# Kernel optimization log

Hardware: AMD Instinct MI355X
Metric: run time of the kernel (lower is better)

The kernel has to match this reference:

```python
import jax, jax.numpy as jnp
import numpy as np

BZ, K, D = 16384, 8192, 512


def setup_inputs() -> dict:
    key = jax.random.key(0)
    kx, ke = jax.random.split(key)
    x = jax.random.normal(kx, (BZ, D), dtype=jnp.float32)
    emb = jax.random.normal(ke, (K, D), dtype=jnp.float32)
    return {"x": x, "emb": emb}


def reference(x, emb):
    x2 = jnp.sum(x * x, axis=1, keepdims=True)           # (bz, 1)
    e2 = jnp.sum(emb * emb, axis=1)                      # (K,)
    dist = x2 + e2[None, :] - 2.0 * jnp.einsum('bd,kd->bk', x, emb)  # (bz, K)
    indices = jnp.argmin(dist, axis=-1)                  # (bz,)
    return jnp.take(emb, indices, axis=0)                # (bz, D)
```

## Files before the change

kernel.cpp:

```cpp
#include <hip/hip_runtime.h>
#include <cfloat>

#define BZ    16384
#define KTOT  8192
#define DD    512
#define KK    512
#define MARGIN 2.0f

typedef unsigned long long u64;
typedef unsigned int       u32;
typedef __attribute__((ext_vector_type(8))) short bf16x8;
typedef __attribute__((ext_vector_type(4))) short bf16x4;
typedef __attribute__((ext_vector_type(4))) float f32x4;

__device__ __forceinline__ u32 f2bf_rne(float f) {
    u32 b = __float_as_uint(f);
    return (b + 0x7FFFu + ((b >> 16) & 1u)) >> 16;
}

__device__ __forceinline__ u64 pack_key(float s, int idx) {
    u32 b   = __float_as_uint(s);
    u32 key = (b & 0x80000000u) ? ~b : (b | 0x80000000u);
    return ((u64)key << 13) | (u32)idx;
}
__device__ __forceinline__ float unpack_val(u64 k) {
    u32 key = (u32)(k >> 13);
    u32 b   = (key & 0x80000000u) ? (key ^ 0x80000000u) : ~key;
    return __uint_as_float(b);
}

__device__ __forceinline__ void gload16(const void* g, void* l) {
    __builtin_amdgcn_global_load_lds(
        (const __attribute__((address_space(1))) void*)g,
        (__attribute__((address_space(3))) void*)l, 16, 0, 0);
}

__global__ void cast_x_kernel(const float* __restrict__ x, ushort* __restrict__ Xs) {
    const size_t base = ((size_t)blockIdx.x * 256 + threadIdx.x) * 8;
    float4 f0 = *(const float4*)(x + base);
    float4 f1 = *(const float4*)(x + base + 4);
    float ff[8] = {f0.x, f0.y, f0.z, f0.w, f1.x, f1.y, f1.z, f1.w};
    bf16x8 vh;
#pragma unroll
    for (int j = 0; j < 8; ++j) vh[j] = (short)f2bf_rne(ff[j]);
    *(bf16x8*)(Xs + base) = vh;
}

__global__ void cast_e_e2_kernel(const float* __restrict__ emb,
                                 ushort* __restrict__ Es, float* __restrict__ e2) {
    const int row  = blockIdx.x * 4 + (threadIdx.x >> 6);
    const int lane = threadIdx.x & 63;
    const float4* p = reinterpret_cast<const float4*>(emb + (size_t)row * DD);
    float4 a = p[lane];
    float4 b = p[lane + 64];
    bf16x4 ha, hb;
    ha[0] = (short)f2bf_rne(a.x); ha[1] = (short)f2bf_rne(a.y);
    ha[2] = (short)f2bf_rne(a.z); ha[3] = (short)f2bf_rne(a.w);
    hb[0] = (short)f2bf_rne(b.x); hb[1] = (short)f2bf_rne(b.y);
    hb[2] = (short)f2bf_rne(b.z); hb[3] = (short)f2bf_rne(b.w);
    ushort* d = Es + (size_t)row * DD;
    *(bf16x4*)(d + lane * 4)       = ha;
    *(bf16x4*)(d + 256 + lane * 4) = hb;
    float s = a.x * a.x + a.y * a.y + a.z * a.z + a.w * a.w
            + b.x * b.x + b.y * b.y + b.z * b.z + b.w * b.w;
#pragma unroll
    for (int off = 32; off >= 1; off >>= 1) s += __shfl_down(s, off, 64);
    if (lane == 0) e2[row] = s;
}

__global__ __launch_bounds__(256) void screen_kernel(
    const ushort* __restrict__ Xs, const ushort* __restrict__ Es,
    const float* __restrict__ e2, u64* __restrict__ cand)
{
    __shared__ __align__(16) ushort As[128 * 32];
    __shared__ __align__(16) ushort Bs[128 * 32];

    const int tid = threadIdx.x;
    const int ns  = blockIdx.x & 7;
    const int rb  = blockIdx.x >> 3;
    const int m0  = rb * 128;
    const int wid = tid >> 6;
    const int l   = tid & 63;
    const int wr  = wid >> 1, wc = wid & 1;
    const int lhi = l >> 4,   llo = l & 15;

    const int sr0 = (wid * 2 + 0) * 16 + (l >> 2);
    const int sr1 = (wid * 2 + 1) * 16 + (l >> 2);
    const int sc  = (l & 3) * 8;

    u64 t2a[16], t2b[16];
#pragma unroll
    for (int i = 0; i < 16; ++i) { t2a[i] = ~0ull; t2b[i] = ~0ull; }

#pragma unroll 1
    for (int nt = 0; nt < 8; ++nt) {
        const int n0 = ns * 1024 + nt * 128;
        f32x4 acc[4][4];
#pragma unroll
        for (int m = 0; m < 4; ++m)
#pragma unroll
            for (int n = 0; n < 4; ++n) acc[m][n] = (f32x4)(0.f);

#pragma unroll 1
        for (int ks = 0; ks < 16; ++ks) {
            const int k0 = ks * 32;
            __syncthreads();
            gload16(Xs + (size_t)(m0 + sr0) * KK + k0 + sc, &As[(wid * 2 + 0) * 512]);
            gload16(Xs + (size_t)(m0 + sr1) * KK + k0 + sc, &As[(wid * 2 + 1) * 512]);
            gload16(Es + (size_t)(n0 + sr0) * KK + k0 + sc, &Bs[(wid * 2 + 0) * 512]);
            gload16(Es + (size_t)(n0 + sr1) * KK + k0 + sc, &Bs[(wid * 2 + 1) * 512]);
            __syncthreads();

            bf16x8 a[4], b[4];
#pragma unroll
            for (int m = 0; m < 4; ++m)
                a[m] = *(const bf16x8*)&As[(wr * 64 + m * 16 + llo) * 32 + lhi * 8];
#pragma unroll
            for (int n = 0; n < 4; ++n)
                b[n] = *(const bf16x8*)&Bs[(wc * 64 + n * 16 + llo) * 32 + lhi * 8];
#pragma unroll
            for (int m = 0; m < 4; ++m)
#pragma unroll
                for (int n = 0; n < 4; ++n)
                    acc[m][n] = __builtin_amdgcn_mfma_f32_16x16x32_bf16(
                        a[m], b[n], acc[m][n], 0, 0, 0);
        }

#pragma unroll
        for (int n = 0; n < 4; ++n) {
            const int col = n0 + wc * 64 + n * 16 + llo;
            const float ee = e2[col];
#pragma unroll
            for (int m = 0; m < 4; ++m)
#pragma unroll
                for (int r = 0; r < 4; ++r) {
                    float s = fmaf(-2.f, acc[m][n][r], ee);
                    u64 k = pack_key(s, col);
                    const int mr = m * 4 + r;
                    if (k < t2a[mr]) { t2b[mr] = t2a[mr]; t2a[mr] = k; }
                    else if (k < t2b[mr]) t2b[mr] = k;
                }
        }
    }

#pragma unroll
    for (int mr = 0; mr < 16; ++mr) {
        u64 a = t2a[mr], b = t2b[mr];
#pragma unroll
        for (int mask = 1; mask < 16; mask <<= 1) {
            u64 oa = __shfl_xor(a, mask, 64);
            u64 ob = __shfl_xor(b, mask, 64);
            u64 hi = a < oa ? oa : a;
            u64 lo2 = b < ob ? b : ob;
            a = a < oa ? a : oa;
            b = hi < lo2 ? hi : lo2;
        }
        if (llo == 0) {
            const int row = m0 + wr * 64 + (mr >> 2) * 16 + lhi * 4 + (mr & 3);
            cand[(size_t)row * 32 + ns * 4 + wc * 2 + 0] = a;
            cand[(size_t)row * 32 + ns * 4 + wc * 2 + 1] = b;
        }
    }
}

__global__ __launch_bounds__(256) void rescore_gather_kernel(
    const float* __restrict__ x, const float* __restrict__ emb,
    const float* __restrict__ e2, const u64* __restrict__ cand,
    float* __restrict__ out)
{
    const int tid = threadIdx.x;
    const int wid = tid >> 6, l = tid & 63;
    const int row = blockIdx.x * 4 + wid;

    u64 c = (l < 32) ? cand[(size_t)row * 32 + l] : ~0ull;
    u64 mn = c;
#pragma unroll
    for (int off = 32; off >= 1; off >>= 1) {
        u64 o = __shfl_xor(mn, off, 64);
        mn = o < mn ? o : mn;
    }
    const float vbest = unpack_val(mn);
    const float v = unpack_val(c);
    const bool amb = (l < 32) && (v <= vbest + MARGIN);
    u64 ball = __ballot(amb);

    int widx;
    if (__popcll(ball) <= 1) {
        widx = (int)(mn & 0x1FFFu);
    } else {
        u64 bestk = ~0ull;
        const float4* xp = (const float4*)(x + (size_t)row * DD);
        while (ball) {
            const int b = __ffsll((unsigned long long)ball) - 1;
            ball &= ball - 1;
            const int ib = __shfl((int)(c & 0x1FFFu), b, 64);
            const float4* ep = (const float4*)(emb + (size_t)ib * DD);
            float4 xa = xp[l],      ea = ep[l];
            float4 xb = xp[l + 64], eb = ep[l + 64];
            float s = xa.x * ea.x + xa.y * ea.y + xa.z * ea.z + xa.w * ea.w
                    + xb.x * eb.x + xb.y * eb.y + xb.z * eb.z + xb.w * eb.w;
#pragma unroll
            for (int off = 32; off >= 1; off >>= 1) s += __shfl_xor(s, off, 64);
            const float d = fmaf(-2.f, s, e2[ib]);
            u64 k = pack_key(d, ib);
            if (k < bestk) bestk = k;
        }
        widx = (int)(bestk & 0x1FFFu);
    }

    const float4* src = (const float4*)(emb + (size_t)widx * DD);
    float4* dst = (float4*)(out + (size_t)row * DD);
    dst[l]      = src[l];
    dst[l + 64] = src[l + 64];
}

#define BM 64
#define BN 64
#define BKf 32
#define NCHUNKf (DD / BKf)
#define NTILESf (KTOT / BN)
#define LDT 68

__global__ void e2_only_kernel(const float* __restrict__ emb, float* __restrict__ e2) {
    const int row  = blockIdx.x * 4 + (threadIdx.x >> 6);
    const int lane = threadIdx.x & 63;
    const float4* p = reinterpret_cast<const float4*>(emb + (size_t)row * DD);
    float4 a = p[lane];
    float4 b = p[lane + 64];
    float s = a.x * a.x + a.y * a.y + a.z * a.z + a.w * a.w
            + b.x * b.x + b.y * b.y + b.z * b.z + b.w * b.w;
#pragma unroll
    for (int off = 32; off >= 1; off >>= 1) s += __shfl_down(s, off, 64);
    if (lane == 0) e2[row] = s;
}

__global__ __launch_bounds__(256) void vq_argmin_kernel(
    const float* __restrict__ x, const float* __restrict__ emb,
    const float* __restrict__ e2, float* __restrict__ out)
{
    __shared__ __align__(16) float xs[2][BKf][LDT];
    __shared__ __align__(16) float es[2][BKf][LDT];
    __shared__ float redv[BM][17];
    __shared__ int   redi[BM][17];
    __shared__ int   idx_s[BM];

    const int tid = threadIdx.x;
    const int tx  = tid & 15;
    const int ty  = tid >> 4;
    const int m0  = blockIdx.x * BM;
    const int srow = tid >> 3;
    const int scol = (tid & 7) << 2;

    const float* xb0 = x + (size_t)(m0 + srow) * DD + scol;
    const float* xb1 = xb0 + (size_t)32 * DD;

    float best[4]; int bidx[4];
#pragma unroll
    for (int i = 0; i < 4; ++i) { best[i] = FLT_MAX; bidx[i] = 0; }

#pragma unroll 1
    for (int nt = 0; nt < NTILESf; ++nt) {
        const int n0 = nt * BN;
        const float* eb0 = emb + (size_t)(n0 + srow) * DD + scol;
        const float* eb1 = eb0 + (size_t)32 * DD;
        float acc[4][4];
#pragma unroll
        for (int i = 0; i < 4; ++i)
#pragma unroll
            for (int j = 0; j < 4; ++j) acc[i][j] = 0.f;
        {
            float4 xa = *(const float4*)(xb0);
            float4 xc = *(const float4*)(xb1);
            float4 ea = *(const float4*)(eb0);
            float4 ec = *(const float4*)(eb1);
#pragma unroll
            for (int i = 0; i < 4; ++i) {
                xs[0][scol + i][srow]      = ((const float*)&xa)[i];
                xs[0][scol + i][srow + 32] = ((const float*)&xc)[i];
                es[0][scol + i][srow]      = ((const float*)&ea)[i];
                es[0][scol + i][srow + 32] = ((const float*)&ec)[i];
            }
        }
        __syncthreads();
        int cur = 0;
#pragma unroll 1
        for (int kk = 1; kk < NCHUNKf; ++kk) {
            float4 nxa = *(const float4*)(xb0 + kk * BKf);
            float4 nxc = *(const float4*)(xb1 + kk * BKf);
            float4 nea = *(const float4*)(eb0 + kk * BKf);
            float4 nec = *(const float4*)(eb1 + kk * BKf);
#pragma unroll
            for (int k = 0; k < BKf; ++k) {
                float4 a = *(const float4*)(&xs[cur][k][ty * 4]);
                float4 b = *(const float4*)(&es[cur][k][tx * 4]);
                acc[0][0] += a.x * b.x; acc[0][1] += a.x * b.y; acc[0][2] += a.x * b.z; acc[0][3] += a.x * b.w;
                acc[1][0] += a.y * b.x; acc[1][1] += a.y * b.y; acc[1][2] += a.y * b.z; acc[1][3] += a.y * b.w;
                acc[2][0] += a.z * b.x; acc[2][1] += a.z * b.y; acc[2][2] += a.z * b.z; acc[2][3] += a.z * b.w;
                acc[3][0] += a.w * b.x; acc[3][1] += a.w * b.y; acc[3][2] += a.w * b.z; acc[3][3] += a.w * b.w;
            }
            const int nb = cur ^ 1;
#pragma unroll
            for (int i = 0; i < 4; ++i) {
                xs[nb][scol + i][srow]      = ((const float*)&nxa)[i];
                xs[nb][scol + i][srow + 32] = ((const float*)&nxc)[i];
                es[nb][scol + i][srow]      = ((const float*)&nea)[i];
                es[nb][scol + i][srow + 32] = ((const float*)&nec)[i];
            }
            __syncthreads();
            cur = nb;
        }
#pragma unroll
        for (int k = 0; k < BKf; ++k) {
            float4 a = *(const float4*)(&xs[cur][k][ty * 4]);
            float4 b = *(const float4*)(&es[cur][k][tx * 4]);
            acc[0][0] += a.x * b.x; acc[0][1] += a.x * b.y; acc[0][2] += a.x * b.z; acc[0][3] += a.x * b.w;
            acc[1][0] += a.y * b.x; acc[1][1] += a.y * b.y; acc[1][2] += a.y * b.z; acc[1][3] += a.y * b.w;
            acc[2][0] += a.z * b.x; acc[2][1] += a.z * b.y; acc[2][2] += a.z * b.z; acc[2][3] += a.z * b.w;
            acc[3][0] += a.w * b.x; acc[3][1] += a.w * b.y; acc[3][2] += a.w * b.z; acc[3][3] += a.w * b.w;
        }
#pragma unroll
        for (int j = 0; j < 4; ++j) {
            const int n  = n0 + tx * 4 + j;
            const float ee = e2[n];
#pragma unroll
            for (int i = 0; i < 4; ++i) {
                float s = ee - 2.0f * acc[i][j];
                if (s < best[i]) { best[i] = s; bidx[i] = n; }
            }
        }
    }
#pragma unroll
    for (int i = 0; i < 4; ++i) {
        redv[ty * 4 + i][tx] = best[i];
        redi[ty * 4 + i][tx] = bidx[i];
    }
    __syncthreads();
    if (tid < BM) {
        float bv = redv[tid][0];
        int   bi = redi[tid][0];
#pragma unroll
        for (int t = 1; t < 16; ++t) {
            float v  = redv[tid][t];
            int   ii = redi[tid][t];
            if (v < bv || (v == bv && ii < bi)) { bv = v; bi = ii; }
        }
        idx_s[tid] = bi;
    }
    __syncthreads();
    for (int c = tid; c < BM * (DD / 4); c += 256) {
        const int r   = c >> 7;
        const int col = (c & 127) << 2;
        const float4 vv = *(const float4*)(emb + (size_t)idx_s[r] * DD + col);
        *(float4*)(out + (size_t)(m0 + r) * DD + col) = vv;
    }
}

extern "C" void kernel_launch(void* const* d_in, const int* in_sizes, int n_in,
                              void* d_out, int out_size, void* d_ws, size_t ws_size,
                              hipStream_t stream) {
    const float* x   = (const float*)d_in[0];
    const float* emb = (const float*)d_in[1];
    float* out = (float*)d_out;

    const size_t XS_BYTES   = (size_t)BZ * KK * 2;
    const size_t ES_BYTES   = (size_t)KTOT * KK * 2;
    const size_t E2_BYTES   = (size_t)KTOT * 4;
    const size_t CAND_BYTES = (size_t)BZ * 32 * 8;
    const size_t NEEDED = XS_BYTES + ES_BYTES + E2_BYTES + CAND_BYTES;

    if (ws_size >= NEEDED) {
        char* base = (char*)d_ws;
        ushort* Xs = (ushort*)base;
        ushort* Es = (ushort*)(base + XS_BYTES);
        float*  e2 = (float*)(base + XS_BYTES + ES_BYTES);
        u64*  cand = (u64*)(base + XS_BYTES + ES_BYTES + E2_BYTES);

        cast_x_kernel<<<(BZ * DD) / (256 * 8), 256, 0, stream>>>(x, Xs);
        cast_e_e2_kernel<<<KTOT / 4, 256, 0, stream>>>(emb, Es, e2);
        screen_kernel<<<(BZ / 128) * 8, 256, 0, stream>>>(Xs, Es, e2, cand);
        rescore_gather_kernel<<<BZ / 4, 256, 0, stream>>>(x, emb, e2, cand, out);
    } else {
        float* e2 = (float*)d_ws;
        e2_only_kernel<<<KTOT / 4, 256, 0, stream>>>(emb, e2);
        vq_argmin_kernel<<<BZ / BM, 256, 0, stream>>>(x, emb, e2, out);
    }
}
```

Before: 379.3 us.

## Double-buffer LDS tiles and track top-2 with biased 32-bit keys

The screening GEMM now double-buffers the A/B LDS tiles. The next k-slice's global-to-LDS loads are issued while the current slice feeds the MFMAs, which leaves one barrier per step instead of two. The per-row top-2 tracking switches from 64-bit packed keys to 32-bit keys. A bias added to e2 keeps distances positive so raw float bits sort correctly, and the low 5 mantissa bits hold the tile position; the column is rebuilt after the cross-lane reduction. This cuts register pressure and compare cost in the epilogue. The mantissa truncation loses precision, so the rescore margin is widened to compensate, and a second e2 buffer is allocated in the workspace.

```diff
diff --git a/kernel.cpp b/kernel.cpp
--- a/kernel.cpp
+++ b/kernel.cpp
@@ -5,7 +5,8 @@
 #define KTOT  8192
 #define DD    512
 #define KK    512
-#define MARGIN 2.0f
+#define MARGIN 2.5f
+#define BIAS  16384.0f
 
 typedef unsigned long long u64;
 typedef unsigned int       u32;
@@ -24,9 +25,7 @@
     return ((u64)key << 13) | (u32)idx;
 }
 __device__ __forceinline__ float unpack_val(u64 k) {
-    u32 key = (u32)(k >> 13);
-    u32 b   = (key & 0x80000000u) ? (key ^ 0x80000000u) : ~key;
-    return __uint_as_float(b);
+    return __uint_as_float((u32)(k >> 13)) - BIAS;
 }
 
 __device__ __forceinline__ void gload16(const void* g, void* l) {
@@ -47,7 +46,8 @@
 }
 
 __global__ void cast_e_e2_kernel(const float* __restrict__ emb,
-                                 ushort* __restrict__ Es, float* __restrict__ e2) {
+                                 ushort* __restrict__ Es, float* __restrict__ e2,
+                                 float* __restrict__ e2b) {
     const int row  = blockIdx.x * 4 + (threadIdx.x >> 6);
     const int lane = threadIdx.x & 63;
     const float4* p = reinterpret_cast<const float4*>(emb + (size_t)row * DD);
@@ -65,15 +65,15 @@
             + b.x * b.x + b.y * b.y + b.z * b.z + b.w * b.w;
 #pragma unroll
     for (int off = 32; off >= 1; off >>= 1) s += __shfl_down(s, off, 64);
-    if (lane == 0) e2[row] = s;
+    if (lane == 0) { e2[row] = s; e2b[row] = s + BIAS; }
 }
 
 __global__ __launch_bounds__(256) void screen_kernel(
     const ushort* __restrict__ Xs, const ushort* __restrict__ Es,
-    const float* __restrict__ e2, u64* __restrict__ cand)
+    const float* __restrict__ e2b, u64* __restrict__ cand)
 {
-    __shared__ __align__(16) ushort As[128 * 32];
-    __shared__ __align__(16) ushort Bs[128 * 32];
+    __shared__ __align__(16) ushort As[2][128 * 32];
+    __shared__ __align__(16) ushort Bs[2][128 * 32];
 
     const int tid = threadIdx.x;
     const int ns  = blockIdx.x & 7;
@@ -88,9 +88,9 @@
     const int sr1 = (wid * 2 + 1) * 16 + (l >> 2);
     const int sc  = (l & 3) * 8;
 
-    u64 t2a[16], t2b[16];
-#pragma unroll
-    for (int i = 0; i < 16; ++i) { t2a[i] = ~0ull; t2b[i] = ~0ull; }
+    u32 ka[16], kb[16];
+#pragma unroll
+    for (int i = 0; i < 16; ++i) { ka[i] = 0xFFFFFFFFu; kb[i] = 0xFFFFFFFFu; }
 
 #pragma unroll 1
     for (int nt = 0; nt < 8; ++nt) {
@@ -101,23 +101,30 @@
 #pragma unroll
             for (int n = 0; n < 4; ++n) acc[m][n] = (f32x4)(0.f);
 
-#pragma unroll 1
+        gload16(Xs + (size_t)(m0 + sr0) * KK + sc, &As[0][(wid * 2 + 0) * 512]);
+        gload16(Xs + (size_t)(m0 + sr1) * KK + sc, &As[0][(wid * 2 + 1) * 512]);
+        gload16(Es + (size_t)(n0 + sr0) * KK + sc, &Bs[0][(wid * 2 + 0) * 512]);
+        gload16(Es + (size_t)(n0 + sr1) * KK + sc, &Bs[0][(wid * 2 + 1) * 512]);
+
+#pragma unroll 2
         for (int ks = 0; ks < 16; ++ks) {
-            const int k0 = ks * 32;
             __syncthreads();
-            gload16(Xs + (size_t)(m0 + sr0) * KK + k0 + sc, &As[(wid * 2 + 0) * 512]);
-            gload16(Xs + (size_t)(m0 + sr1) * KK + k0 + sc, &As[(wid * 2 + 1) * 512]);
-            gload16(Es + (size_t)(n0 + sr0) * KK + k0 + sc, &Bs[(wid * 2 + 0) * 512]);
-            gload16(Es + (size_t)(n0 + sr1) * KK + k0 + sc, &Bs[(wid * 2 + 1) * 512]);
-            __syncthreads();
-
+            const int cur = ks & 1;
+            if (ks < 15) {
+                const int k1 = (ks + 1) * 32;
+                const int nb = cur ^ 1;
+                gload16(Xs + (size_t)(m0 + sr0) * KK + k1 + sc, &As[nb][(wid * 2 + 0) * 512]);
+                gload16(Xs + (size_t)(m0 + sr1) * KK + k1 + sc, &As[nb][(wid * 2 + 1) * 512]);
+                gload16(Es + (size_t)(n0 + sr0) * KK + k1 + sc, &Bs[nb][(wid * 2 + 0) * 512]);
+                gload16(Es + (size_t)(n0 + sr1) * KK + k1 + sc, &Bs[nb][(wid * 2 + 1) * 512]);
+            }
             bf16x8 a[4], b[4];
 #pragma unroll
             for (int m = 0; m < 4; ++m)
-                a[m] = *(const bf16x8*)&As[(wr * 64 + m * 16 + llo) * 32 + lhi * 8];
+                a[m] = *(const bf16x8*)&As[cur][(wr * 64 + m * 16 + llo) * 32 + lhi * 8];
 #pragma unroll
             for (int n = 0; n < 4; ++n)
-                b[n] = *(const bf16x8*)&Bs[(wc * 64 + n * 16 + llo) * 32 + lhi * 8];
+                b[n] = *(const bf16x8*)&Bs[cur][(wc * 64 + n * 16 + llo) * 32 + lhi * 8];
 #pragma unroll
             for (int m = 0; m < 4; ++m)
 #pragma unroll
@@ -128,37 +135,45 @@
 
 #pragma unroll
         for (int n = 0; n < 4; ++n) {
-            const int col = n0 + wc * 64 + n * 16 + llo;
-            const float ee = e2[col];
+            const int col16 = n0 + wc * 64 + n * 16;
+            const float eeC = e2b[col16 + llo];
+            const u32 pos = (u32)(nt * 4 + n);
 #pragma unroll
             for (int m = 0; m < 4; ++m)
 #pragma unroll
                 for (int r = 0; r < 4; ++r) {
-                    float s = fmaf(-2.f, acc[m][n][r], ee);
-                    u64 k = pack_key(s, col);
+                    const float s = fmaf(-2.f, acc[m][n][r], eeC);
+                    const u32 k = (__float_as_uint(s) & 0xFFFFFFE0u) | pos;
                     const int mr = m * 4 + r;
-                    if (k < t2a[mr]) { t2b[mr] = t2a[mr]; t2a[mr] = k; }
-                    else if (k < t2b[mr]) t2b[mr] = k;
+                    const bool c2 = k < kb[mr];
+                    const bool c1 = k < ka[mr];
+                    kb[mr] = c1 ? ka[mr] : (c2 ? k : kb[mr]);
+                    ka[mr] = c1 ? k : ka[mr];
                 }
         }
     }
 
 #pragma unroll
     for (int mr = 0; mr < 16; ++mr) {
-        u64 a = t2a[mr], b = t2b[mr];
+        u64 a = ((u64)ka[mr] << 4) | (u32)llo;
+        u64 b = ((u64)kb[mr] << 4) | (u32)llo;
 #pragma unroll
         for (int mask = 1; mask < 16; mask <<= 1) {
             u64 oa = __shfl_xor(a, mask, 64);
             u64 ob = __shfl_xor(b, mask, 64);
-            u64 hi = a < oa ? oa : a;
+            u64 hi  = a < oa ? oa : a;
             u64 lo2 = b < ob ? b : ob;
             a = a < oa ? a : oa;
             b = hi < lo2 ? hi : lo2;
         }
         if (llo == 0) {
             const int row = m0 + wr * 64 + (mr >> 2) * 16 + lhi * 4 + (mr & 3);
-            cand[(size_t)row * 32 + ns * 4 + wc * 2 + 0] = a;
-            cand[(size_t)row * 32 + ns * 4 + wc * 2 + 1] = b;
+            const u32 k32a = (u32)(a >> 4), la = (u32)a & 15u, pa = k32a & 31u;
+            const u32 k32b = (u32)(b >> 4), lb = (u32)b & 15u, pb = k32b & 31u;
+            const u32 cola = (u32)(ns * 1024) + (pa >> 2) * 128 + (u32)(wc * 64) + (pa & 3u) * 16 + la;
+            const u32 colb = (u32)(ns * 1024) + (pb >> 2) * 128 + (u32)(wc * 64) + (pb & 3u) * 16 + lb;
+            cand[(size_t)row * 32 + ns * 4 + wc * 2 + 0] = ((u64)k32a << 13) | cola;
+            cand[(size_t)row * 32 + ns * 4 + wc * 2 + 1] = ((u64)k32b << 13) | colb;
         }
     }
 }
@@ -366,7 +381,7 @@
     const size_t ES_BYTES   = (size_t)KTOT * KK * 2;
     const size_t E2_BYTES   = (size_t)KTOT * 4;
     const size_t CAND_BYTES = (size_t)BZ * 32 * 8;
-    const size_t NEEDED = XS_BYTES + ES_BYTES + E2_BYTES + CAND_BYTES;
+    const size_t NEEDED = XS_BYTES + ES_BYTES + 2 * E2_BYTES + CAND_BYTES;
 
     if (ws_size >= NEEDED) {
         char* base = (char*)d_ws;
@@ -374,10 +389,11 @@
         ushort* Es = (ushort*)(base + XS_BYTES);
         float*  e2 = (float*)(base + XS_BYTES + ES_BYTES);
         u64*  cand = (u64*)(base + XS_BYTES + ES_BYTES + E2_BYTES);
+        float* e2b = (float*)(base + XS_BYTES + ES_BYTES + E2_BYTES + CAND_BYTES);
 
         cast_x_kernel<<<(BZ * DD) / (256 * 8), 256, 0, stream>>>(x, Xs);
-        cast_e_e2_kernel<<<KTOT / 4, 256, 0, stream>>>(emb, Es, e2);
-        screen_kernel<<<(BZ / 128) * 8, 256, 0, stream>>>(Xs, Es, e2, cand);
+        cast_e_e2_kernel<<<KTOT / 4, 256, 0, stream>>>(emb, Es, e2, e2b);
+        screen_kernel<<<(BZ / 128) * 8, 256, 0, stream>>>(Xs, Es, e2b, cand);
         rescore_gather_kernel<<<BZ / 4, 256, 0, stream>>>(x, emb, e2, cand, out);
     } else {
         float* e2 = (float*)d_ws;
```

New measurement: 462.3 us. 1.22x slower.
